# Kernel tuning notes

Measured on AMD Instinct MI355X. Metric: run time of the kernel, lower is better.

The kernel has to match this reference:

```python
import jax, jax.numpy as jnp
import numpy as np

B, T, C, H = 4, 2048, 1024, 16


def setup_inputs() -> dict:
    key = jax.random.key(0)
    k1, k2, k3 = jax.random.split(key, 3)
    x = jax.random.normal(k1, (B, T, C), dtype=jnp.float32)
    Wqkv = jax.random.normal(k2, (C, 3 * C), dtype=jnp.float32) * 0.02
    bqkv = jnp.zeros((3 * C,), dtype=jnp.float32)
    Wproj = jax.random.normal(k3, (C, C), dtype=jnp.float32) * 0.02
    bproj = jnp.zeros((C,), dtype=jnp.float32)
    return {"x": x, "Wqkv": Wqkv, "bqkv": bqkv, "Wproj": Wproj, "bproj": bproj}


def reference(x, Wqkv, bqkv, Wproj, bproj):
    Bx, Tx, Cx = x.shape
    head = Cx // H
    qkv = x @ Wqkv + bqkv                      # [B,T,3C]
    q, k, v = jnp.split(qkv, 3, axis=-1)
    q = q.reshape(Bx, Tx, H, head)
    k = k.reshape(Bx, Tx, H, head)
    v = v.reshape(Bx, Tx, H, head)
    scale = 1.0 / jnp.sqrt(jnp.asarray(head, dtype=x.dtype))
    scores = jnp.einsum('bqhd,bkhd->bhqk', q, k) * scale   # [B,H,T,T]
    causal = jnp.tril(jnp.ones((Tx, Tx), dtype=bool))       # [T,T]
    neg = jnp.finfo(x.dtype).min
    scores = jnp.where(causal[None, None, :, :], scores, neg)
    probs = jax.nn.softmax(scores, axis=-1)
    y = jnp.einsum('bhqk,bkhd->bqhd', probs, v).reshape(Bx, Tx, Cx)
    return y @ Wproj + bproj
```

## Files before the change

kernel.cpp:

```cpp
#include <hip/hip_runtime.h>
#include <stdint.h>

#define BB 4
#define TT 2048
#define CC 1024
#define HH 16

typedef __bf16 bf16x8 __attribute__((ext_vector_type(8)));
typedef float f32x4 __attribute__((ext_vector_type(4)));
typedef float f32x16 __attribute__((ext_vector_type(16)));
typedef unsigned short ushort8 __attribute__((ext_vector_type(8)));
typedef unsigned short ushort4v __attribute__((ext_vector_type(4)));

__device__ __forceinline__ unsigned short f2b(float f) {
    union { float f; unsigned u; } v; v.f = f;
    unsigned r = v.u + 0x7FFFu + ((v.u >> 16) & 1u);
    return (unsigned short)(r >> 16);
}
__device__ __forceinline__ unsigned pack2(float a, float b) {
    union { float f; unsigned u; } ua, ub; ua.f = a; ub.f = b;
    return __builtin_amdgcn_perm(ub.u + 0x8000u, ua.u + 0x8000u, 0x07060302u);
}
__device__ __forceinline__ float fexp2(float x) {
#if __has_builtin(__builtin_amdgcn_exp2f)
    return __builtin_amdgcn_exp2f(x);
#else
    return exp2f(x);
#endif
}
#define LOG2E 1.4426950408889634f

#define ASYNC16(gp, lp) __builtin_amdgcn_global_load_lds( \
    (const __attribute__((address_space(1))) void*)(gp),  \
    (__attribute__((address_space(3))) void*)(lp), 16, 0, 0)

__global__ __launch_bounds__(256) void k_cast(const float* __restrict__ in,
                                              unsigned short* __restrict__ out, int n) {
    int i = (blockIdx.x * 256 + threadIdx.x) * 4;
    if (i >= n) return;
    float4 v = *(const float4*)(in + i);
    ushort4v o;
    o.x = f2b(v.x); o.y = f2b(v.y); o.z = f2b(v.z); o.w = f2b(v.w);
    *(ushort4v*)(out + i) = o;
}

__global__ __launch_bounds__(256) void k_transpose_bf16(const float* __restrict__ in,
                                                        unsigned short* __restrict__ out,
                                                        int R, int Cc) {
    __shared__ float tile[32][33];
    int bx = blockIdx.x * 32, by = blockIdx.y * 32;
    int tx = threadIdx.x, ty = threadIdx.y;
    for (int i = 0; i < 32; i += 8)
        tile[ty + i][tx] = in[(size_t)(by + ty + i) * Cc + bx + tx];
    __syncthreads();
    for (int i = 0; i < 32; i += 8)
        out[(size_t)(bx + ty + i) * R + by + tx] = f2b(tile[tx][ty + i]);
}

#define QSCALE 0.125f
template <int MODE>
__global__ __launch_bounds__(256) void k_gemm(const unsigned short* __restrict__ A,
                                              const unsigned short* __restrict__ Bt,
                                              const float* __restrict__ bias,
                                              float* __restrict__ outf,
                                              unsigned short* __restrict__ qo,
                                              unsigned short* __restrict__ ko,
                                              unsigned short* __restrict__ vo,
                                              int M, int N, int K) {
    __shared__ unsigned short sm[8704];
    unsigned short* As = sm;
    unsigned short* Bs = sm + 4096;
    const int t = threadIdx.x;
    const int lane = t & 63;
    const int c = lane & 15, qd = lane >> 4;
    const int wave = t >> 6;
    const int wr = (wave >> 1) * 64, wc = (wave & 1) * 64;
    const int bm = blockIdx.x * 128, bn = blockIdx.y * 128;

    f32x4 acc[4][4] = {};

    const unsigned short* Ap = A + (size_t)(bm + (t >> 2)) * K + (t & 3) * 8;
    const unsigned short* Bp = Bt + (size_t)(bn + (t >> 2)) * K + (t & 3) * 8;
    unsigned short* Asw = &As[t * 8];
    unsigned short* Bsw = &Bs[t * 8];

    for (int k0 = 0; k0 < K; k0 += 32) {
        __syncthreads();
        ASYNC16(Ap + k0, Asw);
        ASYNC16(Ap + (size_t)64 * K + k0, Asw + 2048);
        ASYNC16(Bp + k0, Bsw);
        ASYNC16(Bp + (size_t)64 * K + k0, Bsw + 2048);
        __syncthreads();
        bf16x8 af[4], bfr[4];
        for (int i = 0; i < 4; i++)
            af[i] = *(const bf16x8*)&As[(wr + i * 16 + c) * 32 + qd * 8];
        for (int j = 0; j < 4; j++)
            bfr[j] = *(const bf16x8*)&Bs[(wc + j * 16 + c) * 32 + qd * 8];
        for (int i = 0; i < 4; i++)
            for (int j = 0; j < 4; j++)
                acc[i][j] = __builtin_amdgcn_mfma_f32_16x16x32_bf16(af[i], bfr[j], acc[i][j], 0, 0, 0);
    }

    for (int j = 0; j < 4; j++) {
        float bv = bias[bn + wc + j * 16 + c];
        for (int i = 0; i < 4; i++)
            for (int r = 0; r < 4; r++)
                acc[i][j][r] += bv;
    }

    if (MODE == 0) {
        float* smf = (float*)sm;
        for (int p = 0; p < 4; p++) {
            __syncthreads();
            int lr0 = (wr >> 2) + qd * 4;
            for (int j = 0; j < 4; j++) {
                int col = wc + j * 16 + c;
                for (int r = 0; r < 4; r++)
                    smf[(lr0 + r) * 132 + col] = acc[p][j][r];
            }
            __syncthreads();
            for (int op = 0; op < 4; op++) {
                int lr = (t >> 5) + op * 8;
                int ch = (t & 31) * 4;
                float4 v = *(float4*)&smf[lr * 132 + ch];
                int grow = bm + (lr >> 4) * 64 + 16 * p + (lr & 15);
                *(float4*)&outf[(size_t)grow * N + bn + ch] = v;
            }
        }
    } else if (bn < 2048) {
        unsigned short* dst = (bn < 1024) ? qo : ko;
        const int dcol0 = (bn < 1024) ? bn : bn - 1024;
        const float sc = (bn < 1024) ? QSCALE : 1.0f;
        for (int p = 0; p < 2; p++) {
            __syncthreads();
            for (int ii = 0; ii < 2; ii++) {
                int i = 2 * p + ii;
                int lr0 = (wr >> 1) + ii * 16 + qd * 4;
                for (int j = 0; j < 4; j++) {
                    int col = wc + j * 16 + c;
                    for (int r = 0; r < 4; r++)
                        sm[(lr0 + r) * 136 + col] = f2b(acc[i][j][r] * sc);
                }
            }
            __syncthreads();
            for (int op = 0; op < 4; op++) {
                int lr = (t >> 4) + op * 16;
                int ch = (t & 15) * 8;
                ushort8 v = *(ushort8*)&sm[lr * 136 + ch];
                int grow = bm + (lr >> 5) * 64 + 32 * p + (lr & 31);
                *(ushort8*)&dst[(size_t)grow * 1024 + dcol0 + ch] = v;
            }
        }
    } else {
        const int bseg = bm >> 11;
        const int bmt = bm & 2047;
        for (int p = 0; p < 2; p++) {
            __syncthreads();
            for (int jj = 0; jj < 2; jj++) {
                int j = 2 * p + jj;
                int dl = (wc >> 1) + jj * 16 + c;
                for (int i = 0; i < 4; i++) {
                    int tl = wr + i * 16 + qd * 4;
                    ushort4v pk;
                    pk.x = f2b(acc[i][j][0]); pk.y = f2b(acc[i][j][1]);
                    pk.z = f2b(acc[i][j][2]); pk.w = f2b(acc[i][j][3]);
                    *(ushort4v*)&sm[dl * 136 + tl] = pk;
                }
            }
            __syncthreads();
            for (int op = 0; op < 4; op++) {
                int dl = (t >> 4) + op * 16;
                int ch = (t & 15) * 8;
                ushort8 v = *(ushort8*)&sm[dl * 136 + ch];
                int d = (bn - 2048) + (dl >> 5) * 64 + 32 * p + (dl & 31);
                *(ushort8*)&vo[((size_t)bseg * 1024 + d) * 2048 + bmt + ch] = v;
            }
        }
    }
}

__global__ __launch_bounds__(256, 4) void k_attn(const unsigned short* __restrict__ q16,
                                                 const unsigned short* __restrict__ k16,
                                                 const unsigned short* __restrict__ vT16,
                                                 unsigned short* __restrict__ y16) {
    const int h = blockIdx.y, b = blockIdx.z;
    const int qi = (((int)blockIdx.x + h) & 15) ^ ((b & 1) ? 15 : 0);
    __shared__ unsigned short smem[128 * 72];
    unsigned short* q_s = smem;
    unsigned short* k_s = smem;
    unsigned short* vt_s = smem + 64 * 72;
    const int t = threadIdx.x, lane = t & 63, wave = t >> 6;
    const int l31 = lane & 31, hl = lane >> 5;
    const int wq = wave * 32;

    {
        int row = t >> 1, c32 = (t & 1) * 32;
        const unsigned short* src = q16 + ((size_t)(b * TT + qi * 128 + row)) * CC + h * 64 + c32;
        ushort8 v0 = *(const ushort8*)(src);
        ushort8 v1 = *(const ushort8*)(src + 8);
        ushort8 v2 = *(const ushort8*)(src + 16);
        ushort8 v3 = *(const ushort8*)(src + 24);
        *(ushort8*)&q_s[row * 72 + c32] = v0;
        *(ushort8*)&q_s[row * 72 + c32 + 8] = v1;
        *(ushort8*)&q_s[row * 72 + c32 + 16] = v2;
        *(ushort8*)&q_s[row * 72 + c32 + 24] = v3;
    }
    __syncthreads();
    bf16x8 qf[4];
    for (int s = 0; s < 4; s++)
        qf[s] = *(const bf16x8*)&q_s[(wq + l31) * 72 + s * 16 + hl * 8];

    f32x16 oacc[2] = {};
    float m = -3e38f, l = 0.f;
    const int qmaxw = qi * 128 + wq + 31;
    const int qminw = qi * 128 + wq;
    const int qg = qi * 128 + wq + l31;
    const int jn = 2 * qi + 2;
    const unsigned short* kbase = k16 + (size_t)b * TT * CC + h * 64;
    const unsigned short* vbase = vT16 + (((size_t)b * 16 + h) * 64) * TT;

    const int row = t >> 2, c16 = (t & 3) * 16;
    const unsigned short* ksrc = kbase + (size_t)row * CC + c16;
    const unsigned short* vsrc = vbase + (size_t)row * TT + c16;
    ushort8 ka = *(const ushort8*)ksrc, kb = *(const ushort8*)(ksrc + 8);
    ushort8 va = *(const ushort8*)vsrc, vb = *(const ushort8*)(vsrc + 8);

    for (int j = 0; j < jn; j++) {
        __syncthreads();
        *(ushort8*)&k_s[row * 72 + c16] = ka;
        *(ushort8*)&k_s[row * 72 + c16 + 8] = kb;
        *(ushort8*)&vt_s[row * 72 + c16] = va;
        *(ushort8*)&vt_s[row * 72 + c16 + 8] = vb;
        __syncthreads();
        if (j + 1 < jn) {
            const unsigned short* kn = ksrc + (size_t)(j + 1) * 64 * CC;
            const unsigned short* vn = vsrc + (j + 1) * 64;
            ka = *(const ushort8*)kn; kb = *(const ushort8*)(kn + 8);
            va = *(const ushort8*)vn; vb = *(const ushort8*)(vn + 8);
        }
        if (j * 64 > qmaxw) continue;

        f32x16 sacc[2] = {};
        for (int c2 = 0; c2 < 2; c2++)
            for (int s = 0; s < 4; s++) {
                bf16x8 kf = *(const bf16x8*)&k_s[(c2 * 32 + l31) * 72 + s * 16 + hl * 8];
                sacc[c2] = __builtin_amdgcn_mfma_f32_32x32x16_bf16(kf, qf[s], sacc[c2], 0, 0, 0);
            }

        if (j * 64 + 63 > qminw) {
            for (int c2 = 0; c2 < 2; c2++)
                for (int r = 0; r < 16; r++) {
                    int kvg = j * 64 + c2 * 32 + (r & 3) + 8 * (r >> 2) + 4 * hl;
                    if (kvg > qg) sacc[c2][r] = -1e30f;
                }
        }

        float mx = -1e30f;
        for (int c2 = 0; c2 < 2; c2++)
            for (int r = 0; r < 16; r++) mx = fmaxf(mx, sacc[c2][r]);
        mx = fmaxf(mx, __shfl_xor(mx, 32, 64));
        float mn = fmaxf(m, mx);
        float negmnl = -mn * LOG2E;
        float alpha = fexp2(fmaf(m, LOG2E, negmnl));
        m = mn;
        float sum = 0.f;
        unsigned pg[2][4][2];
        for (int c2 = 0; c2 < 2; c2++)
            for (int g = 0; g < 4; g++) {
                float p0 = fexp2(fmaf(sacc[c2][g * 4 + 0], LOG2E, negmnl));
                float p1 = fexp2(fmaf(sacc[c2][g * 4 + 1], LOG2E, negmnl));
                float p2 = fexp2(fmaf(sacc[c2][g * 4 + 2], LOG2E, negmnl));
                float p3 = fexp2(fmaf(sacc[c2][g * 4 + 3], LOG2E, negmnl));
                sum += (p0 + p1) + (p2 + p3);
                pg[c2][g][0] = pack2(p0, p1);
                pg[c2][g][1] = pack2(p2, p3);
            }
        sum += __shfl_xor(sum, 32, 64);
        l = l * alpha + sum;
        if (__ballot(alpha != 1.0f)) {
            for (int c2 = 0; c2 < 2; c2++)
                for (int r = 0; r < 16; r++) oacc[c2][r] *= alpha;
        }

        bf16x8 pf[4];
        for (int c2 = 0; c2 < 2; c2++)
            for (int pr = 0; pr < 2; pr++) {
                unsigned se0 = hl ? pg[c2][2 * pr][0] : pg[c2][2 * pr + 1][0];
                unsigned se1 = hl ? pg[c2][2 * pr][1] : pg[c2][2 * pr + 1][1];
                unsigned r0 = (unsigned)__shfl_xor((int)se0, 32, 64);
                unsigned r1 = (unsigned)__shfl_xor((int)se1, 32, 64);
                union { unsigned u[4]; bf16x8 v; } fr;
                fr.u[0] = hl ? r0 : pg[c2][2 * pr][0];
                fr.u[1] = hl ? r1 : pg[c2][2 * pr][1];
                fr.u[2] = hl ? pg[c2][2 * pr + 1][0] : r0;
                fr.u[3] = hl ? pg[c2][2 * pr + 1][1] : r1;
                pf[c2 * 2 + pr] = fr.v;
            }

        for (int s = 0; s < 4; s++)
            for (int c2o = 0; c2o < 2; c2o++) {
                bf16x8 vf = *(const bf16x8*)&vt_s[(c2o * 32 + l31) * 72 + s * 16 + hl * 8];
                oacc[c2o] = __builtin_amdgcn_mfma_f32_32x32x16_bf16(vf, pf[s], oacc[c2o], 0, 0, 0);
            }
    }

    float rl = 1.0f / l;
    size_t rowb = ((size_t)b * TT + qg) * CC + h * 64;
    for (int c2 = 0; c2 < 2; c2++)
        for (int g = 0; g < 4; g++) {
            ushort4v pk;
            pk.x = f2b(oacc[c2][g * 4 + 0] * rl);
            pk.y = f2b(oacc[c2][g * 4 + 1] * rl);
            pk.z = f2b(oacc[c2][g * 4 + 2] * rl);
            pk.w = f2b(oacc[c2][g * 4 + 3] * rl);
            *(ushort4v*)&y16[rowb + c2 * 32 + g * 8 + hl * 4] = pk;
        }
}

extern "C" void kernel_launch(void* const* d_in, const int* in_sizes, int n_in,
                              void* d_out, int out_size, void* d_ws, size_t ws_size,
                              hipStream_t stream) {
    const float* x     = (const float*)d_in[0];
    const float* Wqkv  = (const float*)d_in[1];
    const float* bqkv  = (const float*)d_in[2];
    const float* Wproj = (const float*)d_in[3];
    const float* bproj = (const float*)d_in[4];
    float* out = (float*)d_out;

    const int M = BB * TT;
    unsigned short* x16    = (unsigned short*)d_ws;
    unsigned short* y16    = x16;
    unsigned short* wqkvT  = x16 + (size_t)M * CC;
    unsigned short* wprojT = wqkvT + (size_t)3 * CC * CC;
    unsigned short* q16    = wprojT + (size_t)CC * CC;
    unsigned short* k16    = q16 + (size_t)M * CC;
    unsigned short* vT16   = k16 + (size_t)M * CC;

    k_cast<<<(M * CC) / 1024, 256, 0, stream>>>(x, x16, M * CC);
    k_transpose_bf16<<<dim3(3 * CC / 32, CC / 32), dim3(32, 8), 0, stream>>>(Wqkv, wqkvT, CC, 3 * CC);
    k_transpose_bf16<<<dim3(CC / 32, CC / 32), dim3(32, 8), 0, stream>>>(Wproj, wprojT, CC, CC);
    k_gemm<1><<<dim3(M / 128, 3 * CC / 128), 256, 0, stream>>>(x16, wqkvT, bqkv, nullptr,
                                                               q16, k16, vT16, M, 3 * CC, CC);
    k_attn<<<dim3(TT / 128, HH, BB), 256, 0, stream>>>(q16, k16, vT16, y16);
    k_gemm<0><<<dim3(M / 128, CC / 128), 256, 0, stream>>>(y16, wprojT, bproj, out,
                                                           nullptr, nullptr, nullptr, M, CC, CC);
}
```

Measured before the change: 274.2 us.

## Add dedicated QKV GEMM kernel with 256x128 tiles and triple-buffered async loads

Replaces the generic MODE-1 GEMM for the QKV projection with a specialized kernel that uses 256x128 block tiles, a three-stage async global-to-LDS pipeline split into two phases per K-step, swizzled LDS layout, and setprio around MFMA bursts. The larger tile increases operand reuse per block and the deeper pipeline aims to hide memory latency behind MFMA work. It uses much more LDS and registers (launch bounds 256,2), halving the grid size along M, which may reduce occupancy and wave-level parallelism. It also adds the bias term in the epilogue.

```diff
diff --git a/kernel.cpp b/kernel.cpp
--- a/kernel.cpp
+++ b/kernel.cpp
@@ -58,6 +58,166 @@
 }
 
 #define QSCALE 0.125f
+
+__global__ __launch_bounds__(256, 2) void k_gemmqkv(const unsigned short* __restrict__ A,
+                                                    const unsigned short* __restrict__ Bt,
+                                                    const float* __restrict__ bias,
+                                                    unsigned short* __restrict__ qo,
+                                                    unsigned short* __restrict__ ko,
+                                                    unsigned short* __restrict__ vo,
+                                                    int M, int N, int K) {
+    __shared__ unsigned short sm[3 * 12288];
+    const int t = threadIdx.x;
+    const int lane = t & 63;
+    const int c = lane & 15, qd = lane >> 4;
+    const int wave = t >> 6;
+    const int wr = wave >> 1, wc = wave & 1;
+    const int bm = blockIdx.x * 256, bn = blockIdx.y * 128;
+
+    f32x4 acc[8][4] = {};
+
+    const int srow = t >> 2;
+    const int sch = (t & 3) ^ ((t >> 3) & 3);
+    const unsigned short* Ap = A + (size_t)(bm + srow) * K + sch * 8;
+    const unsigned short* Bp = Bt + (size_t)(bn + srow) * K + sch * 8;
+    const int fch = qd ^ ((c >> 1) & 3);
+    const int NT = K >> 5;
+
+#define STG_P0(buf, tt_) do {                                              \
+        const unsigned short* ga_ = Ap + (size_t)(tt_) * 32;               \
+        const unsigned short* gb_ = Bp + (size_t)(tt_) * 32;               \
+        ASYNC16(ga_,                  &sm[(buf) * 12288 + t * 8]);         \
+        ASYNC16(ga_ + (size_t)64 * K, &sm[(buf) * 12288 + 2048 + t * 8]);  \
+        ASYNC16(gb_,                  &sm[(buf) * 12288 + 8192 + t * 8]);  \
+    } while (0)
+#define STG_P1(buf, tt_) do {                                              \
+        const unsigned short* ga_ = Ap + (size_t)(tt_) * 32;               \
+        const unsigned short* gb_ = Bp + (size_t)(tt_) * 32;               \
+        ASYNC16(ga_ + (size_t)128 * K, &sm[(buf) * 12288 + 4096 + t * 8]); \
+        ASYNC16(ga_ + (size_t)192 * K, &sm[(buf) * 12288 + 6144 + t * 8]); \
+        ASYNC16(gb_ + (size_t)64 * K,  &sm[(buf) * 12288 + 10240 + t * 8]);\
+    } while (0)
+
+    STG_P0(0, 0); STG_P1(0, 0);
+    STG_P0(1, 1); STG_P1(1, 1);
+    asm volatile("s_waitcnt vmcnt(6)" ::: "memory");
+    __builtin_amdgcn_s_barrier();
+
+    int bc = 0, b1 = 1, bs = 2;
+    for (int tt = 0; tt < NT; ++tt) {
+        const unsigned short* Ab = &sm[bc * 12288];
+        const unsigned short* Bb = &sm[bc * 12288 + 8192];
+        bf16x8 bf_[4], af[4];
+
+        if (tt + 2 < NT) STG_P0(bs, tt + 2);
+#pragma unroll
+        for (int j = 0; j < 4; j++)
+            bf_[j] = *(const bf16x8*)&Bb[(wc * 64 + j * 16 + c) * 32 + fch * 8];
+#pragma unroll
+        for (int i = 0; i < 4; i++)
+            af[i] = *(const bf16x8*)&Ab[(wr * 128 + i * 16 + c) * 32 + fch * 8];
+        __builtin_amdgcn_s_barrier();
+        asm volatile("s_waitcnt lgkmcnt(0)" ::: "memory");
+        __builtin_amdgcn_sched_barrier(0);
+        __builtin_amdgcn_s_setprio(1);
+#pragma unroll
+        for (int i = 0; i < 4; i++)
+#pragma unroll
+            for (int j = 0; j < 4; j++)
+                acc[i][j] = __builtin_amdgcn_mfma_f32_16x16x32_bf16(af[i], bf_[j], acc[i][j], 0, 0, 0);
+        __builtin_amdgcn_s_setprio(0);
+        __builtin_amdgcn_s_barrier();
+
+        if (tt + 2 < NT) STG_P1(bs, tt + 2);
+#pragma unroll
+        for (int i = 0; i < 4; i++)
+            af[i] = *(const bf16x8*)&Ab[(wr * 128 + 64 + i * 16 + c) * 32 + fch * 8];
+        if (tt + 2 < NT) {
+            asm volatile("s_waitcnt vmcnt(6)" ::: "memory");
+        } else if (tt + 1 < NT) {
+            asm volatile("s_waitcnt vmcnt(0)" ::: "memory");
+        }
+        __builtin_amdgcn_s_barrier();
+        asm volatile("s_waitcnt lgkmcnt(0)" ::: "memory");
+        __builtin_amdgcn_sched_barrier(0);
+        __builtin_amdgcn_s_setprio(1);
+#pragma unroll
+        for (int i = 0; i < 4; i++)
+#pragma unroll
+            for (int j = 0; j < 4; j++)
+                acc[i + 4][j] = __builtin_amdgcn_mfma_f32_16x16x32_bf16(af[i], bf_[j], acc[i + 4][j], 0, 0, 0);
+        __builtin_amdgcn_s_setprio(0);
+        __builtin_amdgcn_s_barrier();
+
+        int tmp = bc; bc = b1; b1 = bs; bs = tmp;
+    }
+#undef STG_P0
+#undef STG_P1
+
+#pragma unroll
+    for (int j = 0; j < 4; j++) {
+        float bv = bias[bn + wc * 64 + j * 16 + c];
+#pragma unroll
+        for (int i = 0; i < 8; i++)
+#pragma unroll
+            for (int r = 0; r < 4; r++)
+                acc[i][j][r] += bv;
+    }
+
+    if (bn < 2048) {
+        unsigned short* dst = (bn < 1024) ? qo : ko;
+        const int dcol0 = (bn < 1024) ? bn : bn - 1024;
+        const float sc = (bn < 1024) ? QSCALE : 1.0f;
+        __syncthreads();
+#pragma unroll
+        for (int i = 0; i < 8; i++) {
+            int lr0 = wr * 128 + i * 16 + qd * 4;
+#pragma unroll
+            for (int j = 0; j < 4; j++) {
+                int col = wc * 64 + j * 16 + c;
+#pragma unroll
+                for (int r = 0; r < 4; r++)
+                    sm[(lr0 + r) * 136 + col] = f2b(acc[i][j][r] * sc);
+            }
+        }
+        __syncthreads();
+#pragma unroll
+        for (int op = 0; op < 16; op++) {
+            int cid = op * 256 + t;
+            int lr = cid >> 4;
+            int ch = (cid & 15) * 8;
+            ushort8 v = *(ushort8*)&sm[lr * 136 + ch];
+            *(ushort8*)&dst[(size_t)(bm + lr) * 1024 + dcol0 + ch] = v;
+        }
+    } else {
+        const int bseg = bm >> 11;
+        const int bmt = bm & 2047;
+        __syncthreads();
+#pragma unroll
+        for (int i = 0; i < 8; i++) {
+            int tok = wr * 128 + i * 16 + qd * 4;
+#pragma unroll
+            for (int j = 0; j < 4; j++) {
+                int dl = wc * 64 + j * 16 + c;
+                ushort4v pk;
+                pk.x = f2b(acc[i][j][0]); pk.y = f2b(acc[i][j][1]);
+                pk.z = f2b(acc[i][j][2]); pk.w = f2b(acc[i][j][3]);
+                *(ushort4v*)&sm[dl * 264 + tok] = pk;
+            }
+        }
+        __syncthreads();
+#pragma unroll
+        for (int op = 0; op < 16; op++) {
+            int cid = op * 256 + t;
+            int dl = cid >> 5;
+            int ch = (cid & 31) * 8;
+            ushort8 v = *(ushort8*)&sm[dl * 264 + ch];
+            int d = (bn - 2048) + dl;
+            *(ushort8*)&vo[((size_t)bseg * 1024 + d) * 2048 + bmt + ch] = v;
+        }
+    }
+}
+
 template <int MODE>
 __global__ __launch_bounds__(256) void k_gemm(const unsigned short* __restrict__ A,
                                               const unsigned short* __restrict__ Bt,
@@ -125,55 +285,6 @@
                 float4 v = *(float4*)&smf[lr * 132 + ch];
                 int grow = bm + (lr >> 4) * 64 + 16 * p + (lr & 15);
                 *(float4*)&outf[(size_t)grow * N + bn + ch] = v;
-            }
-        }
-    } else if (bn < 2048) {
-        unsigned short* dst = (bn < 1024) ? qo : ko;
-        const int dcol0 = (bn < 1024) ? bn : bn - 1024;
-        const float sc = (bn < 1024) ? QSCALE : 1.0f;
-        for (int p = 0; p < 2; p++) {
-            __syncthreads();
-            for (int ii = 0; ii < 2; ii++) {
-                int i = 2 * p + ii;
-                int lr0 = (wr >> 1) + ii * 16 + qd * 4;
-                for (int j = 0; j < 4; j++) {
-                    int col = wc + j * 16 + c;
-                    for (int r = 0; r < 4; r++)
-                        sm[(lr0 + r) * 136 + col] = f2b(acc[i][j][r] * sc);
-                }
-            }
-            __syncthreads();
-            for (int op = 0; op < 4; op++) {
-                int lr = (t >> 4) + op * 16;
-                int ch = (t & 15) * 8;
-                ushort8 v = *(ushort8*)&sm[lr * 136 + ch];
-                int grow = bm + (lr >> 5) * 64 + 32 * p + (lr & 31);
-                *(ushort8*)&dst[(size_t)grow * 1024 + dcol0 + ch] = v;
-            }
-        }
-    } else {
-        const int bseg = bm >> 11;
-        const int bmt = bm & 2047;
-        for (int p = 0; p < 2; p++) {
-            __syncthreads();
-            for (int jj = 0; jj < 2; jj++) {
-                int j = 2 * p + jj;
-                int dl = (wc >> 1) + jj * 16 + c;
-                for (int i = 0; i < 4; i++) {
-                    int tl = wr + i * 16 + qd * 4;
-                    ushort4v pk;
-                    pk.x = f2b(acc[i][j][0]); pk.y = f2b(acc[i][j][1]);
-                    pk.z = f2b(acc[i][j][2]); pk.w = f2b(acc[i][j][3]);
-                    *(ushort4v*)&sm[dl * 136 + tl] = pk;
-                }
-            }
-            __syncthreads();
-            for (int op = 0; op < 4; op++) {
-                int dl = (t >> 4) + op * 16;
-                int ch = (t & 15) * 8;
-                ushort8 v = *(ushort8*)&sm[dl * 136 + ch];
-                int d = (bn - 2048) + (dl >> 5) * 64 + 32 * p + (dl & 31);
-                *(ushort8*)&vo[((size_t)bseg * 1024 + d) * 2048 + bmt + ch] = v;
             }
         }
     }
@@ -339,7 +450,7 @@
     k_cast<<<(M * CC) / 1024, 256, 0, stream>>>(x, x16, M * CC);
     k_transpose_bf16<<<dim3(3 * CC / 32, CC / 32), dim3(32, 8), 0, stream>>>(Wqkv, wqkvT, CC, 3 * CC);
     k_transpose_bf16<<<dim3(CC / 32, CC / 32), dim3(32, 8), 0, stream>>>(Wproj, wprojT, CC, CC);
-    k_gemm<1><<<dim3(M / 128, 3 * CC / 128), 256, 0, stream>>>(x16, wqkvT, bqkv, nullptr,
+    k_gemmqkv<<<dim3(M / 256, 3 * CC / 128), 256, 0, stream>>>(x16, wqkvT, bqkv,
                                                                q16, k16, vT16, M, 3 * CC, CC);
     k_attn<<<dim3(TT / 128, HH, BB), 256, 0, stream>>>(q16, k16, vT16, y16);
     k_gemm<0><<<dim3(M / 128, CC / 128), 256, 0, stream>>>(y16, wprojT, bproj, out,
```

Result: faster. 257.7 us (-6.0%).
